# Optimization experiments

Measured on AMD Instinct MI355X. Metric: run time of the kernel, lower is better.

The kernel has to match this reference:

```python
import jax, jax.numpy as jnp
import numpy as np

DIM = 256
NUM_HEADS = 4
HEAD_DIM = DIM // NUM_HEADS
SCALE = HEAD_DIM ** -0.5


def setup_inputs() -> dict:
    key = jax.random.key(0)
    ks = jax.random.split(key, 6)
    B, S = 4, 4096
    x = jax.random.normal(ks[0], (B, S, DIM), dtype=jnp.float32)
    # nn.Linear weights are [out, in]; we store them that way and apply x @ W.T
    wq = jax.random.normal(ks[1], (DIM, DIM), dtype=jnp.float32) * (DIM ** -0.5)
    wk = jax.random.normal(ks[2], (DIM, DIM), dtype=jnp.float32) * (DIM ** -0.5)
    wv = jax.random.normal(ks[3], (DIM, DIM), dtype=jnp.float32) * (DIM ** -0.5)
    wo = jax.random.normal(ks[4], (DIM, DIM), dtype=jnp.float32) * (DIM ** -0.5)
    bo = jax.random.normal(ks[5], (DIM,), dtype=jnp.float32) * 0.02
    return {"x": x, "wq": wq, "wk": wk, "wv": wv, "wo": wo, "bo": bo}


def reference(x, wq, wk, wv, wo, bo):
    B, S, D = x.shape
    H, Hd = NUM_HEADS, HEAD_DIM
    # project and split heads: [B, H, S, Hd]
    q = (x @ wq.T).reshape(B, S, H, Hd).transpose(0, 2, 1, 3)
    k = (x @ wk.T).reshape(B, S, H, Hd).transpose(0, 2, 1, 3)
    v = (x @ wv.T).reshape(B, S, H, Hd).transpose(0, 2, 1, 3)
    attn = jnp.einsum('bhqd,bhkd->bhqk', q, k) * SCALE
    attn = jax.nn.softmax(attn, axis=-1)  # dropout is identity in eval mode
    out = jnp.einsum('bhqk,bhkd->bhqd', attn, v)
    out = out.transpose(0, 2, 1, 3).reshape(B, S, D)
    return out @ wo.T + bo
```

## Files before the change

kernel.cpp:

```cpp
#include <hip/hip_runtime.h>
#include <hip/hip_bf16.h>
#include <stdint.h>

#define DIM    256
#define NH     4
#define HD     64
#define BATCH  4
#define SEQ    4096
#define NTOK   (BATCH*SEQ)

typedef __bf16    bf16_t;
typedef _Float16  f16_t;
typedef _Float16  f16x8  __attribute__((ext_vector_type(8)));
typedef _Float16  f16x4  __attribute__((ext_vector_type(4)));
typedef float     f32x4  __attribute__((ext_vector_type(4)));
typedef float     f32x16 __attribute__((ext_vector_type(16)));
typedef unsigned short u16x8 __attribute__((ext_vector_type(8)));
typedef unsigned int   u32;
typedef u32 u32x2 __attribute__((ext_vector_type(2)));
typedef u32 u32x4 __attribute__((ext_vector_type(4)));

#define MFMA_F16    __builtin_amdgcn_mfma_f32_16x16x32_f16
#define MFMA32_F16  __builtin_amdgcn_mfma_f32_32x32x16_f16

#define QSCALE 0.18033688011112042f

#define WS_XA    ((size_t)0)
#define WS_Q     ((size_t)4194304)
#define WS_K     ((size_t)8388608)
#define WS_VT    ((size_t)12582912)
#define WS_W     ((size_t)16777216)
#define WS_BO    ((size_t)17039360)
#define WS_OATT  WS_XA

__device__ __forceinline__ size_t tiled_idx(int row, int k) {
  return ((size_t)(row >> 4) * 32 + (k >> 3)) * 128 + (row & 15) * 8 + (k & 7);
}

__device__ __forceinline__ int detect_mode(const uint32_t* wq_u32) {
  uint32_t word = wq_u32[(threadIdx.x & 63) * 431 + 17];
  uint32_t b = (word >> 8) & 0x7fu;
  unsigned long long m = __ballot(b >= 0x38u && b <= 0x3fu);
  return (__popcll(m) >= 32) ? 0 : 1;
}

__device__ __forceinline__ f16x8 cvt_chunk(const void* src, size_t elem, int mode) {
  f16x8 r;
  if (mode) {
    const float* s = (const float*)src + elem;
    #pragma unroll
    for (int j = 0; j < 8; ++j) r[j] = (f16_t)s[j];
  } else {
    u16x8 v = *(const u16x8*)((const unsigned short*)src + elem);
    #pragma unroll
    for (int j = 0; j < 8; ++j) r[j] = (f16_t)__uint_as_float(((unsigned)v[j]) << 16);
  }
  return r;
}

__device__ __forceinline__ u32 pkh(float a, float b) {
  auto h = __builtin_amdgcn_cvt_pkrtz(a, b);
  return __builtin_bit_cast(u32, h);
}

__device__ __forceinline__ void swap32(u32& x, u32& y) {
#if __has_builtin(__builtin_amdgcn_permlane32_swap)
  u32x2 r = __builtin_amdgcn_permlane32_swap(x, y, false, false);
  x = r[0]; y = r[1];
#else
  u32 xp = __shfl_xor((int)x, 32), yp = __shfl_xor((int)y, 32);
  const bool h = (threadIdx.x & 32) != 0;
  u32 nx = h ? yp : x;
  u32 ny = h ? y  : xp;
  x = nx; y = ny;
#endif
}

__global__ __launch_bounds__(256) void cvt_all_kernel(
    const void* __restrict__ x,
    const void* __restrict__ wq, const void* __restrict__ wk,
    const void* __restrict__ wv, const void* __restrict__ wo,
    const void* __restrict__ bo,
    f16_t* __restrict__ xA, f16_t* __restrict__ wT,
    float* __restrict__ bof) {
  __shared__ int s_mode;
  if (threadIdx.x < 64) {
    int m = detect_mode((const uint32_t*)wq);
    if (threadIdx.x == 0) s_mode = m;
  }
  __syncthreads();
  const int mode = s_mode;
  const int bid = blockIdx.x;

  if (bid < 2048) {
    int idx = bid * 256 + (int)threadIdx.x;
    int tok = idx >> 5, kc = idx & 31;
    f16x8 r = cvt_chunk(x, (size_t)tok * DIM + kc * 8, mode);
    *(f16x8*)(xA + tiled_idx(tok, kc * 8)) = r;
  } else if (bid < 2176) {
    int idx = (bid - 2048) * 256 + (int)threadIdx.x;
    int which = idx >> 13, local = idx & 8191;
    const void* src = (which == 0) ? wq : (which == 1) ? wk : (which == 2) ? wv : wo;
    int n = local >> 5, kc = local & 31;
    f16x8 r = cvt_chunk(src, (size_t)n * DIM + kc * 8, mode);
    *(f16x8*)(wT + (size_t)which * 65536 + tiled_idx(n, kc * 8)) = r;
  } else {
    int i = threadIdx.x;
    bof[i] = mode ? ((const float*)bo)[i] : (float)((const bf16_t*)bo)[i];
  }
}

__global__ __launch_bounds__(256) void proj_fused_kernel(
    const f16_t* __restrict__ xA, const f16_t* __restrict__ wT,
    f16_t* __restrict__ q, f16_t* __restrict__ kk, f16_t* __restrict__ vt) {
  const int z    = blockIdx.z;
  const f16_t* w = wT + (size_t)z * 65536;
  const int lane = threadIdx.x & 63;
  const int wvi  = threadIdx.x >> 6;
  const int c    = lane & 15;
  const int g    = lane >> 4;

  if (z < 2) {
    const float scale = (z == 0) ? QSCALE : 1.0f;
    const int m0 = blockIdx.x * 64 + wvi * 16;
    const int n0 = blockIdx.y * 64;
    const f16_t* abase = xA + (size_t)(m0 >> 4) * 4096 + c * 8;
    const f16_t* bbase = w + (size_t)(n0 >> 4) * 4096 + c * 8;
    f32x4 acc[4] = {};
    #pragma unroll
    for (int ks = 0; ks < 8; ++ks) {
      const int kc = (ks * 4 + g) * 128;
      f16x8 a = *(const f16x8*)(abase + kc);
      #pragma unroll
      for (int nt = 0; nt < 4; ++nt) {
        f16x8 b = *(const f16x8*)(bbase + (size_t)nt * 4096 + kc);
        acc[nt] = MFMA_F16(a, b, acc[nt], 0, 0, 0);
      }
    }
    if (z == 0) {
      #pragma unroll
      for (int nt = 0; nt < 4; ++nt) {
        const int n = n0 + nt * 16 + c;
        const int h = n >> 6, d = n & 63;
        #pragma unroll
        for (int r = 0; r < 4; ++r) {
          const int tok = m0 + g * 4 + r;
          const int b = tok >> 12, s = tok & 4095;
          q[(size_t)((b * NH + h) * SEQ + s) * HD + d] = (f16_t)(acc[nt][r] * scale);
        }
      }
    } else {
      #pragma unroll
      for (int nt = 0; nt < 4; ++nt) {
        const int n = n0 + nt * 16 + c;
        const int h = n >> 6, d = n & 63;
        #pragma unroll
        for (int r = 0; r < 4; ++r) {
          const int tok = m0 + g * 4 + r;
          const int b = tok >> 12, s = tok & 4095;
          const int kt = s >> 6, row = s & 63;
          const int ch = (d >> 3) ^ (row & 7);
          kk[(size_t)(b * NH + h) * (SEQ * HD) + kt * 4096 + row * 64 + ch * 8 + (d & 7)]
              = (f16_t)acc[nt][r];
        }
      }
    }
  } else {
    const int m0 = blockIdx.y * 64 + wvi * 16;
    const int n0 = blockIdx.x * 64;
    const f16_t* abase = w + (size_t)(m0 >> 4) * 4096 + c * 8;
    const f16_t* bbase = xA + (size_t)(n0 >> 4) * 4096 + c * 8;
    f32x4 acc[4] = {};
    #pragma unroll
    for (int ks = 0; ks < 8; ++ks) {
      const int kc = (ks * 4 + g) * 128;
      f16x8 a = *(const f16x8*)(abase + kc);
      #pragma unroll
      for (int nt = 0; nt < 4; ++nt) {
        f16x8 b = *(const f16x8*)(bbase + (size_t)nt * 4096 + kc);
        acc[nt] = MFMA_F16(a, b, acc[nt], 0, 0, 0);
      }
    }
    #pragma unroll
    for (int nt = 0; nt < 4; ++nt) {
      const int tok = n0 + nt * 16 + c;
      const int b = tok >> 12, s = tok & 4095;
      const int kt = s >> 6, ko = s & 63;
      #pragma unroll
      for (int r = 0; r < 4; ++r) {
        const int vd = m0 + g * 4 + r;
        const int h = vd >> 6, d = vd & 63;
        const int ch = (ko >> 3) ^ (d & 7);
        vt[(size_t)(b * NH + h) * (SEQ * HD) + kt * 4096 + d * 64 + ch * 8 + (ko & 7)]
            = (f16_t)acc[nt][r];
      }
    }
  }
}

__global__ __launch_bounds__(256, 2) void attn_kernel(
    const f16_t* __restrict__ q, const f16_t* __restrict__ kimg,
    const f16_t* __restrict__ vimg, f16_t* __restrict__ o) {
  __shared__ __align__(16) f16_t smem[16896];

  const int tid = threadIdx.x;
  const int l   = tid & 63;
  const int w   = tid >> 6;
  const int wq_ = w & 1;
  const int wk_ = w >> 1;
  const int ql  = l & 31;
  const int hi  = l >> 5;
  const int bh  = blockIdx.x;
  const int q0  = blockIdx.y * 128;

  const f16_t* qb = q + ((size_t)bh * SEQ + q0 + wq_ * 64 + ql) * HD + hi * 8;
  f16x8 qf[2][4];
  #pragma unroll
  for (int qt = 0; qt < 2; ++qt)
    #pragma unroll
    for (int s = 0; s < 4; ++s)
      qf[qt][s] = *(const f16x8*)(qb + (size_t)qt * 32 * HD + s * 16);

  const bool isv = tid >= 128;
  const f16_t* gsrc = (isv ? vimg : kimg) + (size_t)bh * (SEQ * HD) + (tid & 127) * 32;
  f16_t* ldst = smem + (isv ? 4096 : 0) + (tid & 127) * 32;

  const int qx  = ql & 7;
  const int krow = wk_ * 32 + ql;
  int koff[4], voff[2][2];
  #pragma unroll
  for (int s = 0; s < 4; ++s)
    koff[s] = krow * 64 + (((s * 2 + hi) ^ qx) * 8);
  #pragma unroll
  for (int dt = 0; dt < 2; ++dt) {
    const int drow = dt * 32 + ql;
    #pragma unroll
    for (int kb = 0; kb < 2; ++kb)
      voff[dt][kb] = 4096 + drow * 64 + (((wk_ * 4 + kb * 2 + hi) ^ qx) * 8);
  }

  f32x16 acc[2][2] = {};
  float lsum[2] = {0.f, 0.f};

  {
    const uint4* gg = (const uint4*)gsrc;
    uint4* dd = (uint4*)ldst;
    dd[0] = gg[0]; dd[1] = gg[1]; dd[2] = gg[2]; dd[3] = gg[3];
  }
  __syncthreads();

  for (int kt = 0; kt < SEQ / 64; ++kt) {
    const int bufo = (kt & 1) * 8192;
    const bool more = kt < SEQ / 64 - 1;
    uint4 s0, s1, s2, s3;
    if (more) {
      const uint4* gg = (const uint4*)(gsrc + (size_t)(kt + 1) * 4096);
      s0 = gg[0]; s1 = gg[1]; s2 = gg[2]; s3 = gg[3];
    }

    f16x8 kf[4], vf[2][2];
    #pragma unroll
    for (int s = 0; s < 4; ++s)
      kf[s] = *(const f16x8*)(smem + bufo + koff[s]);
    #pragma unroll
    for (int dt = 0; dt < 2; ++dt)
      #pragma unroll
      for (int kb = 0; kb < 2; ++kb)
        vf[dt][kb] = *(const f16x8*)(smem + bufo + voff[dt][kb]);

    f16x8 pf[2][2];
    #pragma unroll
    for (int qt = 0; qt < 2; ++qt) {
      f32x16 st = {};
      #pragma unroll
      for (int s = 0; s < 4; ++s) st = MFMA32_F16(kf[s], qf[qt][s], st, 0, 0, 0);
      float p[16];
      #pragma unroll
      for (int r = 0; r < 16; ++r) p[r] = __builtin_amdgcn_exp2f(st[r]);
      float ls = 0.f;
      #pragma unroll
      for (int r = 0; r < 16; r += 4) ls += (p[r] + p[r + 1]) + (p[r + 2] + p[r + 3]);
      lsum[qt] += ls;
      #pragma unroll
      for (int kb = 0; kb < 2; ++kb) {
        u32 d0 = pkh(p[kb * 8 + 0], p[kb * 8 + 1]);
        u32 d1 = pkh(p[kb * 8 + 2], p[kb * 8 + 3]);
        u32 d2 = pkh(p[kb * 8 + 4], p[kb * 8 + 5]);
        u32 d3 = pkh(p[kb * 8 + 6], p[kb * 8 + 7]);
        swap32(d0, d2);
        swap32(d1, d3);
        u32x4 fd; fd[0] = d0; fd[1] = d1; fd[2] = d2; fd[3] = d3;
        pf[qt][kb] = __builtin_bit_cast(f16x8, fd);
      }
    }

    #pragma unroll
    for (int dt = 0; dt < 2; ++dt)
      #pragma unroll
      for (int qt = 0; qt < 2; ++qt) {
        f32x16 a = acc[dt][qt];
        a = MFMA32_F16(vf[dt][0], pf[qt][0], a, 0, 0, 0);
        a = MFMA32_F16(vf[dt][1], pf[qt][1], a, 0, 0, 0);
        acc[dt][qt] = a;
      }

    if (more) {
      uint4* dd = (uint4*)(ldst + (bufo ^ 8192));
      dd[0] = s0; dd[1] = s1; dd[2] = s2; dd[3] = s3;
    }
    __syncthreads();
  }

  float* lred = (float*)(smem + 16384);
  #pragma unroll
  for (int qt = 0; qt < 2; ++qt) {
    lsum[qt] += __shfl_xor(lsum[qt], 32);
    if (hi == 0) lred[w * 64 + qt * 32 + ql] = lsum[qt];
  }
  float* red = (float*)smem;
  if (wk_ == 1) {
    #pragma unroll
    for (int t = 0; t < 4; ++t) {
      f32x16 a = acc[t >> 1][t & 1];
      #pragma unroll
      for (int qd = 0; qd < 4; ++qd) {
        f32x4 v = { a[qd * 4], a[qd * 4 + 1], a[qd * 4 + 2], a[qd * 4 + 3] };
        *(f32x4*)(red + wq_ * 4096 + (t * 4 + qd) * 256 + l * 4) = v;
      }
    }
  }
  __syncthreads();
  if (wk_ == 0) {
    float inv[2];
    #pragma unroll
    for (int qt = 0; qt < 2; ++qt)
      inv[qt] = 1.0f / (lred[w * 64 + qt * 32 + ql] + lred[(w + 2) * 64 + qt * 32 + ql]);

    const int b = bh >> 2, h = bh & 3;
    #pragma unroll
    for (int dt = 0; dt < 2; ++dt)
      #pragma unroll
      for (int qt = 0; qt < 2; ++qt) {
        const int t = dt * 2 + qt;
        f32x16 a = acc[dt][qt];
        const int tokg = b * SEQ + q0 + wq_ * 64 + qt * 32 + ql;
        const size_t rowbase = (size_t)(tokg >> 4) * 32 * 128 + (tokg & 15) * 8 + hi * 4;
        #pragma unroll
        for (int qd = 0; qd < 4; ++qd) {
          f32x4 v = *(const f32x4*)(red + wq_ * 4096 + (t * 4 + qd) * 256 + l * 4);
          f16x4 ov = { (f16_t)((a[qd * 4 + 0] + v[0]) * inv[qt]),
                       (f16_t)((a[qd * 4 + 1] + v[1]) * inv[qt]),
                       (f16_t)((a[qd * 4 + 2] + v[2]) * inv[qt]),
                       (f16_t)((a[qd * 4 + 3] + v[3]) * inv[qt]) };
          *(f16x4*)(o + rowbase + (size_t)(h * 8 + dt * 4 + qd) * 128) = ov;
        }
      }
  }
}

__global__ __launch_bounds__(256) void out_proj_kernel(
    const f16_t* __restrict__ aA, const f16_t* __restrict__ wT,
    const float* __restrict__ bo, void* __restrict__ outv,
    const void* __restrict__ wq_raw) {
  __shared__ int s_mode;
  if (threadIdx.x < 64) {
    int m = detect_mode((const uint32_t*)wq_raw);
    if (threadIdx.x == 0) s_mode = m;
  }
  __syncthreads();
  const int mode = s_mode;

  const int lane = threadIdx.x & 63;
  const int wv   = threadIdx.x >> 6;
  const int c    = lane & 15;
  const int g    = lane >> 4;
  const int m0   = blockIdx.x * 64 + wv * 16;
  const int n0   = blockIdx.y * 64;

  const f16_t* abase = aA + (size_t)(m0 >> 4) * 4096 + c * 8;
  const f16_t* bbase = wT + (size_t)(n0 >> 4) * 4096 + c * 8;
  f32x4 acc[4] = {};

  #pragma unroll
  for (int ks = 0; ks < 8; ++ks) {
    const int kc = (ks * 4 + g) * 128;
    f16x8 a = *(const f16x8*)(abase + kc);
    #pragma unroll
    for (int nt = 0; nt < 4; ++nt) {
      f16x8 b = *(const f16x8*)(bbase + (size_t)nt * 4096 + kc);
      acc[nt] = MFMA_F16(a, b, acc[nt], 0, 0, 0);
    }
  }

  #pragma unroll
  for (int nt = 0; nt < 4; ++nt) {
    const int n = n0 + nt * 16 + c;
    const float bias = bo[n];
    #pragma unroll
    for (int r = 0; r < 4; ++r) {
      const int tok = m0 + g * 4 + r;
      const float val = acc[nt][r] + bias;
      const size_t idx = (size_t)tok * DIM + n;
      if (mode) ((float*)outv)[idx] = val;
      else      ((bf16_t*)outv)[idx] = (bf16_t)val;
    }
  }
}

extern "C" void kernel_launch(void* const* d_in, const int* in_sizes, int n_in,
                              void* d_out, int out_size, void* d_ws, size_t ws_size,
                              hipStream_t stream) {
  (void)in_sizes; (void)n_in; (void)out_size; (void)ws_size;
  const void* x  = d_in[0];
  const void* wq = d_in[1];
  const void* wk = d_in[2];
  const void* wv = d_in[3];
  const void* wo = d_in[4];
  const void* bo = d_in[5];

  f16_t* ws    = (f16_t*)d_ws;
  f16_t* xA    = ws + WS_XA;
  f16_t* q     = ws + WS_Q;
  f16_t* kk    = ws + WS_K;
  f16_t* vt    = ws + WS_VT;
  f16_t* wT    = ws + WS_W;
  f16_t* woT   = ws + WS_W + 196608;
  float* bof   = (float*)(ws + WS_BO);
  f16_t* oattA = ws + WS_OATT;

  cvt_all_kernel   <<<dim3(2177),      256, 0, stream>>>(x, wq, wk, wv, wo, bo,
                                                         xA, wT, bof);
  proj_fused_kernel<<<dim3(256, 4, 3), 256, 0, stream>>>(xA, wT, q, kk, vt);
  attn_kernel      <<<dim3(16, 32),    256, 0, stream>>>(q, kk, vt, oattA);
  out_proj_kernel  <<<dim3(256, 4),    256, 0, stream>>>(oattA, woT, bof, d_out, wq);
}
```

Baseline: 191.0 us.

## Load K/V fragments directly from global in MFMA-ready layout, drop LDS staging

```diff
diff --git a/kernel.cpp b/kernel.cpp
--- a/kernel.cpp
+++ b/kernel.cpp
@@ -154,14 +154,14 @@
       for (int nt = 0; nt < 4; ++nt) {
         const int n = n0 + nt * 16 + c;
         const int h = n >> 6, d = n & 63;
+        const int sg = d >> 4, hi2 = (d >> 3) & 1, j = d & 7;
         #pragma unroll
         for (int r = 0; r < 4; ++r) {
           const int tok = m0 + g * 4 + r;
           const int b = tok >> 12, s = tok & 4095;
-          const int kt = s >> 6, row = s & 63;
-          const int ch = (d >> 3) ^ (row & 7);
-          kk[(size_t)(b * NH + h) * (SEQ * HD) + kt * 4096 + row * 64 + ch * 8 + (d & 7)]
-              = (f16_t)acc[nt][r];
+          const int kt = s >> 6, h2 = (s >> 5) & 1, row = s & 31;
+          kk[(size_t)(b * NH + h) * (SEQ * HD) + (size_t)kt * 4096 +
+             h2 * 2048 + sg * 512 + hi2 * 256 + row * 8 + j] = (f16_t)acc[nt][r];
         }
       }
     }
@@ -185,13 +185,14 @@
     for (int nt = 0; nt < 4; ++nt) {
       const int tok = n0 + nt * 16 + c;
       const int b = tok >> 12, s = tok & 4095;
-      const int kt = s >> 6, ko = s & 63;
+      const int kt = s >> 6, kin = s & 63;
+      const int h2 = kin >> 5, kb = (kin >> 4) & 1, hiv = (kin >> 3) & 1, jv = kin & 7;
       #pragma unroll
       for (int r = 0; r < 4; ++r) {
         const int vd = m0 + g * 4 + r;
         const int h = vd >> 6, d = vd & 63;
-        const int ch = (ko >> 3) ^ (d & 7);
-        vt[(size_t)(b * NH + h) * (SEQ * HD) + kt * 4096 + d * 64 + ch * 8 + (ko & 7)]
+        vt[(size_t)(b * NH + h) * (SEQ * HD) + (size_t)kt * 4096 +
+           h2 * 2048 + (d >> 5) * 1024 + kb * 512 + hiv * 256 + (d & 31) * 8 + jv]
             = (f16_t)acc[nt][r];
       }
     }
@@ -221,54 +222,35 @@
     for (int s = 0; s < 4; ++s)
       qf[qt][s] = *(const f16x8*)(qb + (size_t)qt * 32 * HD + s * 16);
 
-  const bool isv = tid >= 128;
-  const f16_t* gsrc = (isv ? vimg : kimg) + (size_t)bh * (SEQ * HD) + (tid & 127) * 32;
-  f16_t* ldst = smem + (isv ? 4096 : 0) + (tid & 127) * 32;
-
-  const int qx  = ql & 7;
-  const int krow = wk_ * 32 + ql;
-  int koff[4], voff[2][2];
-  #pragma unroll
-  for (int s = 0; s < 4; ++s)
-    koff[s] = krow * 64 + (((s * 2 + hi) ^ qx) * 8);
-  #pragma unroll
-  for (int dt = 0; dt < 2; ++dt) {
-    const int drow = dt * 32 + ql;
-    #pragma unroll
-    for (int kb = 0; kb < 2; ++kb)
-      voff[dt][kb] = 4096 + drow * 64 + (((wk_ * 4 + kb * 2 + hi) ^ qx) * 8);
-  }
+  const f16_t* kW = kimg + (size_t)bh * (SEQ * HD) + wk_ * 2048 + l * 8;
+  const f16_t* vW = vimg + (size_t)bh * (SEQ * HD) + wk_ * 2048 + l * 8;
 
   f32x16 acc[2][2] = {};
   float lsum[2] = {0.f, 0.f};
 
-  {
-    const uint4* gg = (const uint4*)gsrc;
-    uint4* dd = (uint4*)ldst;
-    dd[0] = gg[0]; dd[1] = gg[1]; dd[2] = gg[2]; dd[3] = gg[3];
-  }
-  __syncthreads();
-
-  for (int kt = 0; kt < SEQ / 64; ++kt) {
-    const int bufo = (kt & 1) * 8192;
-    const bool more = kt < SEQ / 64 - 1;
-    uint4 s0, s1, s2, s3;
-    if (more) {
-      const uint4* gg = (const uint4*)(gsrc + (size_t)(kt + 1) * 4096);
-      s0 = gg[0]; s1 = gg[1]; s2 = gg[2]; s3 = gg[3];
-    }
-
-    f16x8 kf[4], vf[2][2];
-    #pragma unroll
-    for (int s = 0; s < 4; ++s)
-      kf[s] = *(const f16x8*)(smem + bufo + koff[s]);
-    #pragma unroll
-    for (int dt = 0; dt < 2; ++dt)
-      #pragma unroll
-      for (int kb = 0; kb < 2; ++kb)
-        vf[dt][kb] = *(const f16x8*)(smem + bufo + voff[dt][kb]);
-
-    f16x8 pf[2][2];
+  f16x8 kfA[4], vfA[2][2], kfB[4], vfB[2][2];
+
+  #pragma unroll
+  for (int s = 0; s < 4; ++s) kfA[s] = *(const f16x8*)(kW + s * 512);
+  #pragma unroll
+  for (int dt = 0; dt < 2; ++dt)
+    #pragma unroll
+    for (int kb = 0; kb < 2; ++kb)
+      vfA[dt][kb] = *(const f16x8*)(vW + dt * 1024 + kb * 512);
+
+  auto body = [&](f16x8 (&kf)[4], f16x8 (&vf)[2][2],
+                  f16x8 (&kfn)[4], f16x8 (&vfn)[2][2], int kt) {
+    if (kt < SEQ / 64 - 1) {
+      const f16_t* kP = kW + (size_t)(kt + 1) * 4096;
+      const f16_t* vP = vW + (size_t)(kt + 1) * 4096;
+      #pragma unroll
+      for (int s = 0; s < 4; ++s) kfn[s] = *(const f16x8*)(kP + s * 512);
+      #pragma unroll
+      for (int dt = 0; dt < 2; ++dt)
+        #pragma unroll
+        for (int kb = 0; kb < 2; ++kb)
+          vfn[dt][kb] = *(const f16x8*)(vP + dt * 1024 + kb * 512);
+    }
     #pragma unroll
     for (int qt = 0; qt < 2; ++qt) {
       f32x16 st = {};
@@ -281,34 +263,34 @@
       #pragma unroll
       for (int r = 0; r < 16; r += 4) ls += (p[r] + p[r + 1]) + (p[r + 2] + p[r + 3]);
       lsum[qt] += ls;
-      #pragma unroll
-      for (int kb = 0; kb < 2; ++kb) {
-        u32 d0 = pkh(p[kb * 8 + 0], p[kb * 8 + 1]);
-        u32 d1 = pkh(p[kb * 8 + 2], p[kb * 8 + 3]);
-        u32 d2 = pkh(p[kb * 8 + 4], p[kb * 8 + 5]);
-        u32 d3 = pkh(p[kb * 8 + 6], p[kb * 8 + 7]);
-        swap32(d0, d2);
-        swap32(d1, d3);
+      f16x8 pf0, pf1;
+      {
+        u32 d0 = pkh(p[0], p[1]), d1 = pkh(p[2], p[3]);
+        u32 d2 = pkh(p[4], p[5]), d3 = pkh(p[6], p[7]);
+        swap32(d0, d2); swap32(d1, d3);
         u32x4 fd; fd[0] = d0; fd[1] = d1; fd[2] = d2; fd[3] = d3;
-        pf[qt][kb] = __builtin_bit_cast(f16x8, fd);
-      }
-    }
-
-    #pragma unroll
-    for (int dt = 0; dt < 2; ++dt)
-      #pragma unroll
-      for (int qt = 0; qt < 2; ++qt) {
+        pf0 = __builtin_bit_cast(f16x8, fd);
+      }
+      {
+        u32 d0 = pkh(p[8], p[9]),  d1 = pkh(p[10], p[11]);
+        u32 d2 = pkh(p[12], p[13]), d3 = pkh(p[14], p[15]);
+        swap32(d0, d2); swap32(d1, d3);
+        u32x4 fd; fd[0] = d0; fd[1] = d1; fd[2] = d2; fd[3] = d3;
+        pf1 = __builtin_bit_cast(f16x8, fd);
+      }
+      #pragma unroll
+      for (int dt = 0; dt < 2; ++dt) {
         f32x16 a = acc[dt][qt];
-        a = MFMA32_F16(vf[dt][0], pf[qt][0], a, 0, 0, 0);
-        a = MFMA32_F16(vf[dt][1], pf[qt][1], a, 0, 0, 0);
+        a = MFMA32_F16(vf[dt][0], pf0, a, 0, 0, 0);
+        a = MFMA32_F16(vf[dt][1], pf1, a, 0, 0, 0);
         acc[dt][qt] = a;
       }
-
-    if (more) {
-      uint4* dd = (uint4*)(ldst + (bufo ^ 8192));
-      dd[0] = s0; dd[1] = s1; dd[2] = s2; dd[3] = s3;
-    }
-    __syncthreads();
+    }
+  };
+
+  for (int kt = 0; kt < SEQ / 64; kt += 2) {
+    body(kfA, vfA, kfB, vfB, kt);
+    body(kfB, vfB, kfA, vfA, kt + 1);
   }
 
   float* lred = (float*)(smem + 16384);
@@ -344,7 +326,7 @@
         const int t = dt * 2 + qt;
         f32x16 a = acc[dt][qt];
         const int tokg = b * SEQ + q0 + wq_ * 64 + qt * 32 + ql;
-        const size_t rowbase = (size_t)(tokg >> 4) * 32 * 128 + (tokg & 15) * 8 + hi * 4;
+        const size_t rowbase = (size_t)(tokg >> 4) * 4096 + (tokg & 15) * 8 + hi * 4;
         #pragma unroll
         for (int qd = 0; qd < 4; ++qd) {
           f32x4 v = *(const f32x4*)(red + wq_ * 4096 + (t * 4 + qd) * 256 + l * 4);
```

After: 179.9 us. 1.06x faster.
